# Performance work log

Measured on AMD Instinct MI355X. Metric: run time of the kernel, lower is better.

Reference implementation:

```python
import jax, jax.numpy as jnp
import numpy as np

NUM_TOKENS = 1024  # max_num_tokens = ori_indexes.max()+1; fixed for jit (indexes drawn in [0,1024))


def setup_inputs() -> dict:
    key = jax.random.key(0)
    k1, k2 = jax.random.split(key)
    hidden = jax.random.normal(k1, (8, 2048, 768), dtype=jnp.float32)
    ori_indexes = jnp.sort(
        jax.random.randint(k2, (8, 2048), 0, NUM_TOKENS, dtype=jnp.int64), axis=-1
    )
    return {"hidden": hidden, "ori_indexes": ori_indexes}


def reference(hidden, ori_indexes):
    # mode='mean': sum sub-token vectors per original token, divide by count (clamped >=1).
    # Equivalent to the torch mask+bmm path, but as a direct segment reduction.
    def agg_one(h, idx):  # h: [S, D], idx: [S]
        summed = jax.ops.segment_sum(h, idx, num_segments=NUM_TOKENS)            # [T, D]
        counts = jax.ops.segment_sum(jnp.ones(idx.shape, h.dtype), idx,
                                     num_segments=NUM_TOKENS)                    # [T]
        return summed / jnp.clip(counts, 1.0)[:, None]
    return jax.vmap(agg_one)(hidden, ori_indexes)  # [B, T, D]
```

## Files before the change

kernel.cpp:

```cpp
#include <hip/hip_runtime.h>
#include <hip/hip_bf16.h>


#define SGA_B 8
#define SGA_S 2048
#define SGA_D 768
#define SGA_T 1024
#define SGA_NV (SGA_D / 4)

typedef float f32x4 __attribute__((ext_vector_type(4)));

__global__ __launch_bounds__(256) void sga_segmean_kernel(
    const float* __restrict__ hidden,
    const int* __restrict__ idx,
    float* __restrict__ out) {
    const int wid = threadIdx.x >> 6;
    const int lane = threadIdx.x & 63;

    const int w = ((blockIdx.x & 7) << 8) | ((int)blockIdx.x >> 3);
    const int b = w >> 8;
    const int t = ((w & 255) << 2) | wid;

    const int* __restrict__ ib = idx + b * SGA_S;

    const int p1 = ib[lane << 5];
    const int ka = __builtin_popcountll(__ballot(p1 < t));
    const int kb = __builtin_popcountll(__ballot(p1 < t + 1));
    const int base_a = ka ? ((ka - 1) << 5) : 0;
    const int base_b = kb ? ((kb - 1) << 5) : 0;

    const int ia = base_a + lane;
    const int pa = ib[ia < SGA_S ? ia : (SGA_S - 1)];
    const int s0 = base_a +
        __builtin_popcountll(__ballot(ia < SGA_S && pa < t));
    int s1;
    if (base_b == base_a) {
        s1 = base_b + __builtin_popcountll(__ballot(ia < SGA_S && pa < t + 1));
    } else {
        const int ibx = base_b + lane;
        const int pb = ib[ibx < SGA_S ? ibx : (SGA_S - 1)];
        s1 = base_b + __builtin_popcountll(__ballot(ibx < SGA_S && pb < t + 1));
    }

    const f32x4* __restrict__ hbase =
        reinterpret_cast<const f32x4*>(hidden) + (size_t)b * SGA_S * SGA_NV + lane;

    f32x4 a0 = (f32x4)0.f, a1 = (f32x4)0.f, a2 = (f32x4)0.f;
    int s = s0;
    for (; s + 1 < s1; s += 2) {
        const f32x4* r0 = hbase + (size_t)s * SGA_NV;
        const f32x4* r1 = r0 + SGA_NV;
        f32x4 v00 = __builtin_nontemporal_load(r0);
        f32x4 v01 = __builtin_nontemporal_load(r0 + 64);
        f32x4 v02 = __builtin_nontemporal_load(r0 + 128);
        f32x4 v10 = __builtin_nontemporal_load(r1);
        f32x4 v11 = __builtin_nontemporal_load(r1 + 64);
        f32x4 v12 = __builtin_nontemporal_load(r1 + 128);
        a0 += v00; a1 += v01; a2 += v02;
        a0 += v10; a1 += v11; a2 += v12;
    }
    if (s < s1) {
        const f32x4* rp = hbase + (size_t)s * SGA_NV;
        a0 += __builtin_nontemporal_load(rp);
        a1 += __builtin_nontemporal_load(rp + 64);
        a2 += __builtin_nontemporal_load(rp + 128);
    }

    const int cnt = s1 - s0;
    const float inv = (cnt > 0) ? (1.0f / (float)cnt) : 0.0f;
    a0 *= inv; a1 *= inv; a2 *= inv;

    f32x4* __restrict__ o =
        reinterpret_cast<f32x4*>(out) + ((size_t)b * SGA_T + t) * SGA_NV + lane;
    __builtin_nontemporal_store(a0, o);
    __builtin_nontemporal_store(a1, o + 64);
    __builtin_nontemporal_store(a2, o + 128);
}

extern "C" void kernel_launch(void* const* d_in, const int* in_sizes, int n_in,
                              void* d_out, int out_size, void* d_ws, size_t ws_size,
                              hipStream_t stream) {
    const float* hidden = (const float*)d_in[0];
    const int* idx = (const int*)d_in[1];
    float* out = (float*)d_out;

    dim3 grid(SGA_B * SGA_T / 4, 1, 1);
    sga_segmean_kernel<<<grid, dim3(256, 1, 1), 0, stream>>>(hidden, idx, out);
}
```

Baseline: 17.81 us.

## Split each segment's rows across two waves and combine via LDS

Each output token is now handled by a pair of wavefronts. Each wave sums half of the segment's rows, then the partial sums are combined through shared memory before the mean is written. The grid doubles so each block covers two tokens instead of four. This raises memory-level parallelism and shortens per-wave serial load chains. The cost is a __syncthreads, LDS traffic, and duplicated index searches across the two waves.

```diff
diff --git a/kernel.cpp b/kernel.cpp
--- a/kernel.cpp
+++ b/kernel.cpp
@@ -16,10 +16,12 @@
     float* __restrict__ out) {
     const int wid = threadIdx.x >> 6;
     const int lane = threadIdx.x & 63;
+    const int pair = wid >> 1;
+    const int h = wid & 1;
 
-    const int w = ((blockIdx.x & 7) << 8) | ((int)blockIdx.x >> 3);
-    const int b = w >> 8;
-    const int t = ((w & 255) << 2) | wid;
+    const int u = ((blockIdx.x & 7) << 9) | ((int)blockIdx.x >> 3);
+    const int b = u >> 9;
+    const int t = (((u & 511) << 1) | pair);
 
     const int* __restrict__ ib = idx + b * SGA_S;
 
@@ -42,39 +44,51 @@
         s1 = base_b + __builtin_popcountll(__ballot(ibx < SGA_S && pb < t + 1));
     }
 
+    const int n = s1 - s0;
+    const int mid = s0 + ((n + 1) >> 1);
+    const int r0 = h ? mid : s0;
+    const int r1 = h ? s1 : mid;
+
     const f32x4* __restrict__ hbase =
         reinterpret_cast<const f32x4*>(hidden) + (size_t)b * SGA_S * SGA_NV + lane;
 
     f32x4 a0 = (f32x4)0.f, a1 = (f32x4)0.f, a2 = (f32x4)0.f;
-    int s = s0;
-    for (; s + 1 < s1; s += 2) {
-        const f32x4* r0 = hbase + (size_t)s * SGA_NV;
-        const f32x4* r1 = r0 + SGA_NV;
-        f32x4 v00 = __builtin_nontemporal_load(r0);
-        f32x4 v01 = __builtin_nontemporal_load(r0 + 64);
-        f32x4 v02 = __builtin_nontemporal_load(r0 + 128);
-        f32x4 v10 = __builtin_nontemporal_load(r1);
-        f32x4 v11 = __builtin_nontemporal_load(r1 + 64);
-        f32x4 v12 = __builtin_nontemporal_load(r1 + 128);
+    int s = r0;
+    for (; s + 1 < r1; s += 2) {
+        const f32x4* q0 = hbase + (size_t)s * SGA_NV;
+        const f32x4* q1 = q0 + SGA_NV;
+        f32x4 v00 = __builtin_nontemporal_load(q0);
+        f32x4 v01 = __builtin_nontemporal_load(q0 + 64);
+        f32x4 v02 = __builtin_nontemporal_load(q0 + 128);
+        f32x4 v10 = __builtin_nontemporal_load(q1);
+        f32x4 v11 = __builtin_nontemporal_load(q1 + 64);
+        f32x4 v12 = __builtin_nontemporal_load(q1 + 128);
         a0 += v00; a1 += v01; a2 += v02;
         a0 += v10; a1 += v11; a2 += v12;
     }
-    if (s < s1) {
-        const f32x4* rp = hbase + (size_t)s * SGA_NV;
-        a0 += __builtin_nontemporal_load(rp);
-        a1 += __builtin_nontemporal_load(rp + 64);
-        a2 += __builtin_nontemporal_load(rp + 128);
+    if (s < r1) {
+        const f32x4* qp = hbase + (size_t)s * SGA_NV;
+        a0 += __builtin_nontemporal_load(qp);
+        a1 += __builtin_nontemporal_load(qp + 64);
+        a2 += __builtin_nontemporal_load(qp + 128);
     }
 
-    const int cnt = s1 - s0;
-    const float inv = (cnt > 0) ? (1.0f / (float)cnt) : 0.0f;
-    a0 *= inv; a1 *= inv; a2 *= inv;
-
-    f32x4* __restrict__ o =
-        reinterpret_cast<f32x4*>(out) + ((size_t)b * SGA_T + t) * SGA_NV + lane;
-    __builtin_nontemporal_store(a0, o);
-    __builtin_nontemporal_store(a1, o + 64);
-    __builtin_nontemporal_store(a2, o + 128);
+    __shared__ float lds[2][SGA_D];
+    f32x4* L = reinterpret_cast<f32x4*>(lds[pair]) + lane;
+    if (h) {
+        L[0] = a0; L[64] = a1; L[128] = a2;
+    }
+    __syncthreads();
+    if (!h) {
+        a0 += L[0]; a1 += L[64]; a2 += L[128];
+        const float inv = (n > 0) ? (1.0f / (float)n) : 0.0f;
+        a0 *= inv; a1 *= inv; a2 *= inv;
+        f32x4* __restrict__ o =
+            reinterpret_cast<f32x4*>(out) + ((size_t)b * SGA_T + t) * SGA_NV + lane;
+        __builtin_nontemporal_store(a0, o);
+        __builtin_nontemporal_store(a1, o + 64);
+        __builtin_nontemporal_store(a2, o + 128);
+    }
 }
 
 extern "C" void kernel_launch(void* const* d_in, const int* in_sizes, int n_in,
@@ -84,6 +98,6 @@
     const int* idx = (const int*)d_in[1];
     float* out = (float*)d_out;
 
-    dim3 grid(SGA_B * SGA_T / 4, 1, 1);
+    dim3 grid(SGA_B * SGA_T / 2, 1, 1);
     sga_segmean_kernel<<<grid, dim3(256, 1, 1), 0, stream>>>(hidden, idx, out);
 }
```

Result: slower. 18.39 us (+3.3%).
